# Kernel optimization log

Measured on AMD Instinct MI355X. Metric: run time of the kernel, lower is better.

The kernel has to match this reference:

```python
import jax, jax.numpy as jnp
import numpy as np

NUM_HEADS = 16
NEG_INF = -1e9  # matches torch source's -1000000000.0 additive mask
ROPE_BASE = 10000.0


def _rope(t):
    """Rotary position embedding, half-rotation form. t: [B, H, S, D]."""
    D = t.shape[-1]
    S = t.shape[2]
    inv_freq = 1.0 / (ROPE_BASE ** (jnp.arange(0, D, 2, dtype=jnp.float32) / D))  # [D/2]
    pos = jnp.arange(S, dtype=jnp.float32)
    freqs = pos[:, None] * inv_freq[None, :]          # [S, D/2]
    cos = jnp.cos(freqs)[None, None]                  # [1,1,S,D/2]
    sin = jnp.sin(freqs)[None, None]
    t1, t2 = t[..., : D // 2], t[..., D // 2 :]
    return jnp.concatenate([t1 * cos - t2 * sin, t1 * sin + t2 * cos], axis=-1)


def setup_inputs() -> dict:
    key = jax.random.key(0)
    kx, kq, kk, kv, ko = jax.random.split(key, 5)
    B, S, Dm = 2, 2048, 1024
    w_scale = 0.02
    return {
        "x": jax.random.normal(kx, (B, S, Dm), dtype=jnp.float32),
        "attention_mask": jnp.ones((B, S), dtype=jnp.float32),
        "Wq": jax.random.normal(kq, (Dm, Dm), dtype=jnp.float32) * w_scale,
        "Wk": jax.random.normal(kk, (Dm, Dm), dtype=jnp.float32) * w_scale,
        "Wv": jax.random.normal(kv, (Dm, Dm), dtype=jnp.float32) * w_scale,
        "Wo": jax.random.normal(ko, (Dm, Dm), dtype=jnp.float32) * w_scale,
    }


def reference(x, attention_mask, Wq, Wk, Wv, Wo):
    B, S, Dm = x.shape
    H = NUM_HEADS
    Hd = Dm // H

    def to_heads(t):  # [B,S,Dm] -> [B,H,S,Hd]
        return t.reshape(B, S, H, Hd).transpose(0, 2, 1, 3)

    q = _rope(to_heads(x @ Wq))
    k = _rope(to_heads(x @ Wk))
    v = to_heads(x @ Wv)

    scaling = 1.0 / np.sqrt(Hd).astype(np.float32)
    scores = jnp.einsum("bhqd,bhkd->bhqk", q, k) * scaling  # [B,H,S,S]

    # causal additive mask (triu of -1e9 above diagonal), as in apply_masking
    causal = jnp.triu(jnp.full((S, S), NEG_INF, dtype=scores.dtype), k=1)
    # padding mask: (1 - mask) * -1e9 broadcast to [B,1,1,S]
    amask = (1.0 - attention_mask)[:, None, None, :] * NEG_INF
    scores = scores + causal[None, None] + amask

    weights = jax.nn.softmax(scores, axis=-1)
    out = jnp.einsum("bhqk,bhkd->bhqd", weights, v)  # [B,H,S,Hd]
    out = out.transpose(0, 2, 1, 3).reshape(B, S, Dm)
    return out @ Wo
```

## Files before the change

kernel.cpp:

```cpp
#include <hip/hip_runtime.h>

typedef unsigned short u16;
typedef unsigned int u32;
typedef __attribute__((ext_vector_type(8))) short short8;
typedef __attribute__((ext_vector_type(4))) short s4v;
typedef __attribute__((ext_vector_type(4))) float f32x4;

#define S_LEN 2048
#define NH 16
#define HD 64
#define DM 1024

#if __has_builtin(__builtin_amdgcn_mfma_f32_16x16x16_bf16)
#define MFMA_K16(a, b, c) __builtin_amdgcn_mfma_f32_16x16x16_bf16(a, b, c, 0, 0, 0)
#else
#define MFMA_K16(a, b, c) __builtin_amdgcn_mfma_f32_16x16x16bf16_1k(a, b, c, 0, 0, 0)
#endif

__device__ __forceinline__ u16 f2bf(float f) {
    union { float f; u32 u; } v; v.f = f;
    u32 u = v.u;
    u32 r = u + 0x7fffu + ((u >> 16) & 1u);
    return (u16)(r >> 16);
}
__device__ __forceinline__ float bf2f(u16 h) {
    union { u32 u; float f; } v; v.u = ((u32)h) << 16;
    return v.f;
}

__device__ __forceinline__ u32 cvtpk_bf16(float lo, float hi) {
    u32 r;
    asm("v_cvt_pk_bf16_f32 %0, %1, %2" : "=v"(r) : "v"(lo), "v"(hi));
    return r;
}

__device__ __forceinline__ void load_lds16(const u16* g, u16* l) {
    __builtin_amdgcn_global_load_lds((const __attribute__((address_space(1))) void*)g,
                                     (__attribute__((address_space(3))) void*)l, 16, 0, 0);
}

__global__ __launch_bounds__(256) void cvt_bf16(const float* __restrict__ in, u16* __restrict__ out, int n) {
    int i = (blockIdx.x * 256 + threadIdx.x) * 4;
    if (i < n) {
        float4 v = *(const float4*)(in + i);
        ushort4 o;
        o.x = f2bf(v.x); o.y = f2bf(v.y); o.z = f2bf(v.z); o.w = f2bf(v.w);
        *(ushort4*)(out + i) = o;
    }
}

__global__ __launch_bounds__(256) void transpose_w4(const float* __restrict__ W0, const float* __restrict__ W1,
                                                    const float* __restrict__ W2, const float* __restrict__ W3,
                                                    u16* __restrict__ T0, u16* __restrict__ T1,
                                                    u16* __restrict__ T2, u16* __restrict__ T3) {
    __shared__ float tile[32][33];
    int z = blockIdx.z;
    const float* W = (z == 0) ? W0 : (z == 1) ? W1 : (z == 2) ? W2 : W3;
    u16* Wt = (z == 0) ? T0 : (z == 1) ? T1 : (z == 2) ? T2 : T3;
    int tx = threadIdx.x, ty = threadIdx.y;
    int k0 = blockIdx.y * 32, n0 = blockIdx.x * 32;
    #pragma unroll
    for (int j = 0; j < 32; j += 8)
        tile[ty + j][tx] = W[(size_t)(k0 + ty + j) * DM + n0 + tx];
    __syncthreads();
    #pragma unroll
    for (int j = 0; j < 32; j += 8)
        Wt[(size_t)(n0 + ty + j) * DM + k0 + tx] = f2bf(tile[tx][ty + j]);
}

template<int MODE, int NI>
__global__ __launch_bounds__(256) void gemm128(const u16* __restrict__ A, const u16* __restrict__ Bt,
                                               u16* __restrict__ Qh, u16* __restrict__ Kh,
                                               u16* __restrict__ Vh, float* __restrict__ Cf) {
    __shared__ u16 Al[128 * 32];
    __shared__ u16 Bl[NI * 32 * 32];
    const int K = DM;
    int tid = threadIdx.x;
    int wave = tid >> 6, lane = tid & 63, g = lane >> 4, ln = lane & 15;
    int wm = (wave >> 1) * 64, wn = (wave & 1) * (NI * 16);
    size_t mb0 = (size_t)blockIdx.y * 128, nb0 = (size_t)blockIdx.x * (NI * 32);

    f32x4 acc[4][NI];
    #pragma unroll
    for (int i = 0; i < 4; i++)
        #pragma unroll
        for (int j = 0; j < NI; j++)
            acc[i][j] = (f32x4){0.f, 0.f, 0.f, 0.f};

    const u16* Ag = A + (mb0 + wave * 32 + (lane >> 2)) * K + (lane & 3) * 8;
    u16* Alw = Al + wave * 1024;
    const u16* Bg;
    u16* Blw;
    if (NI == 4) {
        Bg = Bt + (nb0 + wave * 32 + (lane >> 2)) * K + (lane & 3) * 8;
        Blw = Bl + wave * 1024;
    } else {
        Bg = Bt + (nb0 + wave * 16 + (lane >> 2)) * K + (lane & 3) * 8;
        Blw = Bl + wave * 512;
    }

    for (int k0 = 0; k0 < K; k0 += 32) {
        __syncthreads();
        #pragma unroll
        for (int c = 0; c < 2; c++)
            load_lds16(Ag + (size_t)c * 16 * K + k0, Alw + c * 512);
        if (NI == 4) {
            #pragma unroll
            for (int c = 0; c < 2; c++)
                load_lds16(Bg + (size_t)c * 16 * K + k0, Blw + c * 512);
        } else {
            load_lds16(Bg + k0, Blw);
        }
        __syncthreads();
        short8 af[4], bf[NI];
        #pragma unroll
        for (int i = 0; i < 4; i++)
            af[i] = *(const short8*)&Al[(wm + i * 16 + ln) * 32 + g * 8];
        #pragma unroll
        for (int i = 0; i < NI; i++)
            bf[i] = *(const short8*)&Bl[(wn + i * 16 + ln) * 32 + g * 8];
        #pragma unroll
        for (int mi = 0; mi < 4; mi++)
            #pragma unroll
            for (int ni = 0; ni < NI; ni++)
                acc[mi][ni] = __builtin_amdgcn_mfma_f32_16x16x32_bf16(af[mi], bf[ni], acc[mi][ni], 0, 0, 0);
    }

    if (MODE == 1) {
        #pragma unroll
        for (int mi = 0; mi < 4; mi++)
            #pragma unroll
            for (int ni = 0; ni < NI; ni++)
                #pragma unroll
                for (int r = 0; r < 4; r++) {
                    int m = (int)mb0 + wm + mi * 16 + g * 4 + r;
                    int n = (int)nb0 + wn + ni * 16 + ln;
                    Cf[(size_t)m * DM + n] = acc[mi][ni][r];
                }
    } else {
        int nbase = (int)nb0 + wn;
        int which = nbase >> 10;
        int h = (nbase & (DM - 1)) >> 6;
        if (which < 2) {
            u16* dst = (which == 0) ? Qh : Kh;
            float inv0 = exp2f(-0.4152408746976557f * (float)ln);
            float inv1 = exp2f(-0.4152408746976557f * (float)(16 + ln));
            #pragma unroll
            for (int mi = 0; mi < 4; mi++) {
                #pragma unroll
                for (int r = 0; r < 4; r++) {
                    int m = (int)mb0 + wm + mi * 16 + g * 4 + r;
                    int b = m >> 11, s = m & (S_LEN - 1);
                    float fs = (float)s;
                    float sn0, cs0, sn1, cs1;
                    __sincosf(fs * inv0, &sn0, &cs0);
                    __sincosf(fs * inv1, &sn1, &cs1);
                    float a0 = acc[mi][0][r], a1 = acc[mi][1][r];
                    float a2 = acc[mi][2][r], a3 = acc[mi][3][r];
                    size_t base = ((size_t)(b * NH + h) * S_LEN + s) * HD;
                    dst[base + ln]      = f2bf(a0 * cs0 - a2 * sn0);
                    dst[base + 16 + ln] = f2bf(a1 * cs1 - a3 * sn1);
                    dst[base + 32 + ln] = f2bf(a0 * sn0 + a2 * cs0);
                    dst[base + 48 + ln] = f2bf(a1 * sn1 + a3 * cs1);
                }
            }
        } else {
            #pragma unroll
            for (int mi = 0; mi < 4; mi++) {
                #pragma unroll
                for (int r = 0; r < 4; r++) {
                    int m = (int)mb0 + wm + mi * 16 + g * 4 + r;
                    int b = m >> 11, s = m & (S_LEN - 1);
                    size_t base = ((size_t)(b * NH + h) * S_LEN + s) * HD;
                    #pragma unroll
                    for (int ni = 0; ni < 4; ni++)
                        Vh[base + ni * 16 + ln] = f2bf(acc[mi][ni][r]);
                }
            }
        }
    }
}

__global__ __launch_bounds__(256) void vtrans(const u16* __restrict__ Vh, u16* __restrict__ Vt) {
    __shared__ u16 t[64][70];
    int tid = threadIdx.x;
    int s0 = blockIdx.x * 64, bh = blockIdx.y;
    int r = tid >> 2, c = (tid & 3) * 8;
    const u16* src = Vh + ((size_t)bh * S_LEN + s0) * HD;
    *(short8*)&t[r][c]      = *(const short8*)(src + (size_t)r * HD + c);
    *(short8*)&t[r][c + 32] = *(const short8*)(src + (size_t)r * HD + c + 32);
    __syncthreads();
    u16* dst = Vt + ((size_t)bh * HD + r) * S_LEN + s0;
    short8 o0, o1;
    #pragma unroll
    for (int j = 0; j < 8; j++) {
        o0[j] = (short)t[c + j][r];
        o1[j] = (short)t[c + 32 + j][r];
    }
    *(short8*)(dst + c)      = o0;
    *(short8*)(dst + c + 32) = o1;
}

__global__ __launch_bounds__(512, 4) void flash_kernel(const u16* __restrict__ Qh, const u16* __restrict__ Kh,
                                                       const u16* __restrict__ Vt, const float* __restrict__ amask,
                                                       u16* __restrict__ Op0, u16* __restrict__ Op1,
                                                       u16* __restrict__ Op2, u16* __restrict__ Op3,
                                                       float* __restrict__ L0, float* __restrict__ L1,
                                                       float* __restrict__ L2, float* __restrict__ L3) {
    __shared__ u16 Kl[2][64 * 64];
    __shared__ u16 Vl[2][64 * 64];
    __shared__ float Ml[2][64];
    int tid = threadIdx.x;
    int wave = tid >> 6, lane = tid & 63, g = lane >> 4, ln = lane & 15;
    int qblk = 15 - ((int)blockIdx.x >> 2);
    int sp = blockIdx.x & 3;
    int bh = blockIdx.y;
    int b = bh >> 4, h = bh & (NH - 1);
    int q0 = qblk * 128 + wave * 16;
    int qv = q0 + ln;
    const u16* Qb = Qh + (size_t)bh * (S_LEN * HD);
    const u16* Kb = Kh + (size_t)bh * (S_LEN * HD);
    const u16* Vb = Vt + (size_t)bh * (S_LEN * HD);
    const float* am = amask + b * S_LEN;

    short8 qa0 = *(const short8*)(Qb + (size_t)(q0 + ln) * HD + g * 8);
    short8 qa1 = *(const short8*)(Qb + (size_t)(q0 + ln) * HD + 32 + g * 8);

    f32x4 O[4];
    #pragma unroll
    for (int i = 0; i < 4; i++) O[i] = (f32x4){0.f, 0.f, 0.f, 0.f};
    float lsum = 0.f;
    const float SCL = 0.125f * 1.4426950408889634f;
    const float MSCL = -1.4426950408889634e9f;

    int T = 2 * qblk + 2;
    int srow = tid >> 3, scid = tid & 7, s7 = srow & 7;
    int stoff = srow * 64 + ((scid ^ s7) * 8);
    const u16* KgP = Kb + (size_t)srow * HD + scid * 8;
    const u16* VgP = Vb + (size_t)srow * S_LEN + scid * 8;
    bool vswap = (wave & 1);

    int l7 = ln & 7;
    int kc0 = (g ^ l7) * 8;
    int kc1 = ((4 + g) ^ l7) * 8;
    int rbq = ln * 64;
    int vcoff[4];
    #pragma unroll
    for (int n0 = 0; n0 < 4; n0++)
        vcoff[n0] = (((n0 * 2 + (g >> 1)) ^ l7) * 8) + ((((g & 1) ^ (ln >> 3)) & 1) * 4);

    short8 kR = *(const short8*)(KgP + (size_t)(sp * 64) * HD);
    short8 vR = *(const short8*)(VgP + sp * 64);
    float mR = 0.f;
    if (tid < 64) mR = (1.0f - am[sp * 64 + tid]) * MSCL;
    int cur = 0;

    for (int kt = sp; kt < T; kt += 4) {
        int kbase = kt * 64;
        short8 vS = vR;
        if (vswap) vS = __builtin_shufflevector(vR, vR, 4, 5, 6, 7, 0, 1, 2, 3);
        *(short8*)(Kl[cur] + stoff) = kR;
        *(short8*)(Vl[cur] + stoff) = vS;
        if (tid < 64) Ml[cur][tid] = mR;
        __syncthreads();

        if (kt + 4 < T) {
            kR = *(const short8*)(KgP + (size_t)(kbase + 256) * HD);
            vR = *(const short8*)(VgP + (kbase + 256));
            if (tid < 64) mR = (1.0f - am[kbase + 256 + tid]) * MSCL;
        }

        const u16* Klc = Kl[cur];
        const u16* Vlc = Vl[cur];
        bool needmask = (kbase + 63 > q0);
        u32 pk[4][2];

        #pragma unroll
        for (int n0 = 0; n0 < 4; n0++) {
            const u16* kr = Klc + (n0 * 16) * 64 + rbq;
            short8 kb0 = *(const short8*)(kr + kc0);
            short8 kb1 = *(const short8*)(kr + kc1);
            f32x4 sv = (f32x4){0.f, 0.f, 0.f, 0.f};
            sv = __builtin_amdgcn_mfma_f32_16x16x32_bf16(kb0, qa0, sv, 0, 0, 0);
            sv = __builtin_amdgcn_mfma_f32_16x16x32_bf16(kb1, qa1, sv, 0, 0, 0);
            f32x4 mkv = *(f32x4*)&Ml[cur][n0 * 16 + g * 4];
            int keyb = kbase + n0 * 16 + g * 4;
            float p[4];
            #pragma unroll
            for (int r = 0; r < 4; r++) {
                float s2 = sv[r] * SCL + mkv[r];
                if (needmask && (keyb + r > qv)) s2 = -1.0e9f;
                p[r] = exp2f(s2);
                lsum += p[r];
            }
            pk[n0][0] = cvtpk_bf16(p[0], p[1]);
            pk[n0][1] = cvtpk_bf16(p[2], p[3]);
        }

        __builtin_amdgcn_s_setprio(1);
        #pragma unroll
        for (int t = 0; t < 4; t++) {
            const u16* vr = Vlc + (t * 16) * 64 + rbq;
            #pragma unroll
            for (int n0 = 0; n0 < 4; n0++) {
                s4v va = *(const s4v*)(vr + vcoff[n0]);
                union { u32 u[2]; s4v v; } pb;
                pb.u[0] = pk[n0][0];
                pb.u[1] = pk[n0][1];
                O[t] = MFMA_K16(va, pb.v, O[t]);
            }
        }
        __builtin_amdgcn_s_setprio(0);
        cur ^= 1;
    }

    lsum += __shfl_xor(lsum, 16, 64);
    lsum += __shfl_xor(lsum, 32, 64);
    u16* Od = (sp == 0) ? Op0 : (sp == 1) ? Op1 : (sp == 2) ? Op2 : Op3;
    float* Ld = (sp == 0) ? L0 : (sp == 1) ? L1 : (sp == 2) ? L2 : L3;
    if (lane < 16) Ld[(size_t)bh * S_LEN + q0 + ln] = lsum;
    size_t obase = (size_t)bh * (HD * S_LEN) + q0 + ln;
    #pragma unroll
    for (int t = 0; t < 4; t++)
        #pragma unroll
        for (int r = 0; r < 4; r++)
            Od[obase + (size_t)(t * 16 + g * 4 + r) * S_LEN] = f2bf(O[t][r]);
}

__global__ __launch_bounds__(256) void flash_reduce(const u16* __restrict__ Op0, const u16* __restrict__ Op1,
                                                    const u16* __restrict__ Op2, const u16* __restrict__ Op3,
                                                    const float* __restrict__ L0, const float* __restrict__ L1,
                                                    const float* __restrict__ L2, const float* __restrict__ L3,
                                                    u16* __restrict__ attn) {
    __shared__ float t[64][65];
    int tid = threadIdx.x;
    int qt = blockIdx.x, bh = blockIdx.y;
    int b = bh >> 4, h = bh & (NH - 1);
    #pragma unroll
    for (int it = 0; it < 2; it++) {
        int idx = tid + it * 256;
        int d = idx >> 3, c = (idx & 7) * 8;
        size_t off = (size_t)bh * (HD * S_LEN) + (size_t)d * S_LEN + qt * 64 + c;
        short8 a0 = *(const short8*)(Op0 + off);
        short8 a1 = *(const short8*)(Op1 + off);
        short8 a2 = *(const short8*)(Op2 + off);
        short8 a3 = *(const short8*)(Op3 + off);
        #pragma unroll
        for (int j = 0; j < 8; j++)
            t[d][c + j] = bf2f((u16)a0[j]) + bf2f((u16)a1[j]) + bf2f((u16)a2[j]) + bf2f((u16)a3[j]);
    }
    __syncthreads();
    int qr = tid >> 2, dc = (tid & 3) * 16;
    int qg = qt * 64 + qr;
    size_t li = (size_t)bh * S_LEN + qg;
    float inv = 1.0f / (L0[li] + L1[li] + L2[li] + L3[li]);
    short8 o0, o1;
    #pragma unroll
    for (int j = 0; j < 8; j++) {
        o0[j] = (short)f2bf(t[dc + j][qr] * inv);
        o1[j] = (short)f2bf(t[dc + 8 + j][qr] * inv);
    }
    u16* dst = attn + ((size_t)b * S_LEN + qg) * DM + h * HD + dc;
    *(short8*)dst = o0;
    *(short8*)(dst + 8) = o1;
}

extern "C" void kernel_launch(void* const* d_in, const int* in_sizes, int n_in,
                              void* d_out, int out_size, void* d_ws, size_t ws_size,
                              hipStream_t stream) {
    const float* x     = (const float*)d_in[0];
    const float* amask = (const float*)d_in[1];
    const float* Wq    = (const float*)d_in[2];
    const float* Wk    = (const float*)d_in[3];
    const float* Wv    = (const float*)d_in[4];
    const float* Wo    = (const float*)d_in[5];
    float* out = (float*)d_out;
    char* ws = (char*)d_ws;

    u16* x_bf   = (u16*)(ws);
    u16* Op1    = (u16*)(ws);
    u16* Wqkv_t = (u16*)(ws + 8388608);
    float* L0   = (float*)(ws + 8388608);
    float* L1   = (float*)(ws + 8650752);
    float* L2   = (float*)(ws + 8912896);
    float* L3   = (float*)(ws + 9175040);
    u16* Wo_t   = (u16*)(ws + 14680064);
    u16* Qh     = (u16*)(ws + 16777216);
    u16* Kh     = (u16*)(ws + 25165824);
    u16* Vt     = (u16*)(ws + 33554432);
    u16* attnF  = (u16*)(ws + 33554432);
    u16* Vh     = (u16*)(ws + 41943040);
    u16* Op0    = (u16*)(ws + 41943040);
    u16* Op2    = (u16*)d_out;
    u16* Op3    = (u16*)d_out + 4194304;

    cvt_bf16<<<4096, 256, 0, stream>>>(x, x_bf, 2 * S_LEN * DM);

    transpose_w4<<<dim3(32, 32, 4), dim3(32, 8), 0, stream>>>(
        Wq, Wk, Wv, Wo, Wqkv_t, Wqkv_t + 1048576, Wqkv_t + 2097152, Wo_t);

    gemm128<0, 4><<<dim3(24, 32), 256, 0, stream>>>(x_bf, Wqkv_t, Qh, Kh, Vh, nullptr);

    vtrans<<<dim3(32, 2 * NH), 256, 0, stream>>>(Vh, Vt);

    flash_kernel<<<dim3(64, 2 * NH), 512, 0, stream>>>(Qh, Kh, Vt, amask,
                                                       Op0, Op1, Op2, Op3, L0, L1, L2, L3);

    flash_reduce<<<dim3(32, 2 * NH), 256, 0, stream>>>(Op0, Op1, Op2, Op3,
                                                       L0, L1, L2, L3, attnF);

    gemm128<1, 2><<<dim3(16, 32), 256, 0, stream>>>(attnF, Wo_t, nullptr, nullptr, nullptr, out);
}
```

Baseline: 225.0 us.

## Double queries per wave in flash kernel and precompute padding mask

Each wave now processes 32 query rows instead of 16, so every K/V tile staged in LDS feeds twice as many MFMAs. The block's query tile grows to 256 and the grid halves, and waves whose rows all sit above a key tile skip it under the causal mask. The padding-mask transform moves into vtrans, which writes it to a global buffer read directly by the flash kernel, removing the per-tile LDS mask staging. This raises register pressure (launch bounds drop from 4 to 3 blocks per CU) and leaves fewer blocks, with more causal imbalance within each block.

```diff
diff --git a/kernel.cpp b/kernel.cpp
--- a/kernel.cpp
+++ b/kernel.cpp
@@ -10,6 +10,7 @@
 #define NH 16
 #define HD 64
 #define DM 1024
+#define MSCL_C (-1.4426950408889634e9f)
 
 #if __has_builtin(__builtin_amdgcn_mfma_f32_16x16x16_bf16)
 #define MFMA_K16(a, b, c) __builtin_amdgcn_mfma_f32_16x16x16_bf16(a, b, c, 0, 0, 0)
@@ -181,10 +182,15 @@
     }
 }
 
-__global__ __launch_bounds__(256) void vtrans(const u16* __restrict__ Vh, u16* __restrict__ Vt) {
+__global__ __launch_bounds__(256) void vtrans(const u16* __restrict__ Vh, u16* __restrict__ Vt,
+                                              const float* __restrict__ amask, float* __restrict__ Mg) {
     __shared__ u16 t[64][70];
     int tid = threadIdx.x;
     int s0 = blockIdx.x * 64, bh = blockIdx.y;
+    if (bh == 0) {
+        int idx = blockIdx.x * 256 + tid;
+        if (idx < 2 * S_LEN) Mg[idx] = (1.0f - amask[idx]) * MSCL_C;
+    }
     int r = tid >> 2, c = (tid & 3) * 8;
     const u16* src = Vh + ((size_t)bh * S_LEN + s0) * HD;
     *(short8*)&t[r][c]      = *(const short8*)(src + (size_t)r * HD + c);
@@ -201,39 +207,39 @@
     *(short8*)(dst + c + 32) = o1;
 }
 
-__global__ __launch_bounds__(512, 4) void flash_kernel(const u16* __restrict__ Qh, const u16* __restrict__ Kh,
-                                                       const u16* __restrict__ Vt, const float* __restrict__ amask,
+__global__ __launch_bounds__(512, 3) void flash_kernel(const u16* __restrict__ Qh, const u16* __restrict__ Kh,
+                                                       const u16* __restrict__ Vt, const float* __restrict__ Mg,
                                                        u16* __restrict__ Op0, u16* __restrict__ Op1,
                                                        u16* __restrict__ Op2, u16* __restrict__ Op3,
                                                        float* __restrict__ L0, float* __restrict__ L1,
                                                        float* __restrict__ L2, float* __restrict__ L3) {
     __shared__ u16 Kl[2][64 * 64];
     __shared__ u16 Vl[2][64 * 64];
-    __shared__ float Ml[2][64];
     int tid = threadIdx.x;
     int wave = tid >> 6, lane = tid & 63, g = lane >> 4, ln = lane & 15;
-    int qblk = 15 - ((int)blockIdx.x >> 2);
+    int qblk = 7 - ((int)blockIdx.x >> 2);
     int sp = blockIdx.x & 3;
     int bh = blockIdx.y;
-    int b = bh >> 4, h = bh & (NH - 1);
-    int q0 = qblk * 128 + wave * 16;
-    int qv = q0 + ln;
+    int b = bh >> 4;
+    int q0 = qblk * 256 + wave * 32;
+    int qvA = q0 + ln, qvB = q0 + 16 + ln;
     const u16* Qb = Qh + (size_t)bh * (S_LEN * HD);
     const u16* Kb = Kh + (size_t)bh * (S_LEN * HD);
     const u16* Vb = Vt + (size_t)bh * (S_LEN * HD);
-    const float* am = amask + b * S_LEN;
+    const float* Mb = Mg + b * S_LEN;
 
     short8 qa0 = *(const short8*)(Qb + (size_t)(q0 + ln) * HD + g * 8);
     short8 qa1 = *(const short8*)(Qb + (size_t)(q0 + ln) * HD + 32 + g * 8);
-
-    f32x4 O[4];
-    #pragma unroll
-    for (int i = 0; i < 4; i++) O[i] = (f32x4){0.f, 0.f, 0.f, 0.f};
-    float lsum = 0.f;
+    short8 qb0 = *(const short8*)(Qb + (size_t)(q0 + 16 + ln) * HD + g * 8);
+    short8 qb1 = *(const short8*)(Qb + (size_t)(q0 + 16 + ln) * HD + 32 + g * 8);
+
+    f32x4 O[8];
+    #pragma unroll
+    for (int i = 0; i < 8; i++) O[i] = (f32x4){0.f, 0.f, 0.f, 0.f};
+    float lsa = 0.f, lsb = 0.f;
     const float SCL = 0.125f * 1.4426950408889634f;
-    const float MSCL = -1.4426950408889634e9f;
-
-    int T = 2 * qblk + 2;
+
+    int T = 4 * qblk + 4;
     int srow = tid >> 3, scid = tid & 7, s7 = srow & 7;
     int stoff = srow * 64 + ((scid ^ s7) * 8);
     const u16* KgP = Kb + (size_t)srow * HD + scid * 8;
@@ -251,8 +257,6 @@
 
     short8 kR = *(const short8*)(KgP + (size_t)(sp * 64) * HD);
     short8 vR = *(const short8*)(VgP + sp * 64);
-    float mR = 0.f;
-    if (tid < 64) mR = (1.0f - am[sp * 64 + tid]) * MSCL;
     int cur = 0;
 
     for (int kt = sp; kt < T; kt += 4) {
@@ -261,70 +265,94 @@
         if (vswap) vS = __builtin_shufflevector(vR, vR, 4, 5, 6, 7, 0, 1, 2, 3);
         *(short8*)(Kl[cur] + stoff) = kR;
         *(short8*)(Vl[cur] + stoff) = vS;
-        if (tid < 64) Ml[cur][tid] = mR;
         __syncthreads();
 
         if (kt + 4 < T) {
             kR = *(const short8*)(KgP + (size_t)(kbase + 256) * HD);
             vR = *(const short8*)(VgP + (kbase + 256));
-            if (tid < 64) mR = (1.0f - am[kbase + 256 + tid]) * MSCL;
         }
 
-        const u16* Klc = Kl[cur];
-        const u16* Vlc = Vl[cur];
-        bool needmask = (kbase + 63 > q0);
-        u32 pk[4][2];
-
-        #pragma unroll
-        for (int n0 = 0; n0 < 4; n0++) {
-            const u16* kr = Klc + (n0 * 16) * 64 + rbq;
-            short8 kb0 = *(const short8*)(kr + kc0);
-            short8 kb1 = *(const short8*)(kr + kc1);
-            f32x4 sv = (f32x4){0.f, 0.f, 0.f, 0.f};
-            sv = __builtin_amdgcn_mfma_f32_16x16x32_bf16(kb0, qa0, sv, 0, 0, 0);
-            sv = __builtin_amdgcn_mfma_f32_16x16x32_bf16(kb1, qa1, sv, 0, 0, 0);
-            f32x4 mkv = *(f32x4*)&Ml[cur][n0 * 16 + g * 4];
-            int keyb = kbase + n0 * 16 + g * 4;
-            float p[4];
-            #pragma unroll
-            for (int r = 0; r < 4; r++) {
-                float s2 = sv[r] * SCL + mkv[r];
-                if (needmask && (keyb + r > qv)) s2 = -1.0e9f;
-                p[r] = exp2f(s2);
-                lsum += p[r];
+        if (kbase <= q0 + 31) {
+            const u16* Klc = Kl[cur];
+            const u16* Vlc = Vl[cur];
+            f32x4 mk[4];
+            #pragma unroll
+            for (int n0 = 0; n0 < 4; n0++)
+                mk[n0] = *(const f32x4*)(Mb + kbase + n0 * 16 + g * 4);
+            bool nmA = (kbase + 63 > q0);
+            bool nmB = (kbase + 63 > q0 + 16);
+            u32 pkA[4][2], pkB[4][2];
+
+            #pragma unroll
+            for (int n0 = 0; n0 < 4; n0++) {
+                const u16* kr = Klc + (n0 * 16) * 64 + rbq;
+                short8 kb0 = *(const short8*)(kr + kc0);
+                short8 kb1 = *(const short8*)(kr + kc1);
+                f32x4 sva = (f32x4){0.f, 0.f, 0.f, 0.f};
+                sva = __builtin_amdgcn_mfma_f32_16x16x32_bf16(kb0, qa0, sva, 0, 0, 0);
+                sva = __builtin_amdgcn_mfma_f32_16x16x32_bf16(kb1, qa1, sva, 0, 0, 0);
+                f32x4 svb = (f32x4){0.f, 0.f, 0.f, 0.f};
+                svb = __builtin_amdgcn_mfma_f32_16x16x32_bf16(kb0, qb0, svb, 0, 0, 0);
+                svb = __builtin_amdgcn_mfma_f32_16x16x32_bf16(kb1, qb1, svb, 0, 0, 0);
+                int keyb = kbase + n0 * 16 + g * 4;
+                float pa[4], pb[4];
+                #pragma unroll
+                for (int r = 0; r < 4; r++) {
+                    float s2 = sva[r] * SCL + mk[n0][r];
+                    if (nmA && (keyb + r > qvA)) s2 = -1.0e9f;
+                    pa[r] = exp2f(s2);
+                    lsa += pa[r];
+                }
+                #pragma unroll
+                for (int r = 0; r < 4; r++) {
+                    float s2 = svb[r] * SCL + mk[n0][r];
+                    if (nmB && (keyb + r > qvB)) s2 = -1.0e9f;
+                    pb[r] = exp2f(s2);
+                    lsb += pb[r];
+                }
+                pkA[n0][0] = cvtpk_bf16(pa[0], pa[1]);
+                pkA[n0][1] = cvtpk_bf16(pa[2], pa[3]);
+                pkB[n0][0] = cvtpk_bf16(pb[0], pb[1]);
+                pkB[n0][1] = cvtpk_bf16(pb[2], pb[3]);
             }
-            pk[n0][0] = cvtpk_bf16(p[0], p[1]);
-            pk[n0][1] = cvtpk_bf16(p[2], p[3]);
+
+            __builtin_amdgcn_s_setprio(1);
+            #pragma unroll
+            for (int t = 0; t < 4; t++) {
+                const u16* vr = Vlc + (t * 16) * 64 + rbq;
+                #pragma unroll
+                for (int n0 = 0; n0 < 4; n0++) {
+                    s4v va = *(const s4v*)(vr + vcoff[n0]);
+                    union { u32 u[2]; s4v v; } pba, pbb;
+                    pba.u[0] = pkA[n0][0]; pba.u[1] = pkA[n0][1];
+                    pbb.u[0] = pkB[n0][0]; pbb.u[1] = pkB[n0][1];
+                    O[t]     = MFMA_K16(va, pba.v, O[t]);
+                    O[4 + t] = MFMA_K16(va, pbb.v, O[4 + t]);
+                }
+            }
+            __builtin_amdgcn_s_setprio(0);
         }
-
-        __builtin_amdgcn_s_setprio(1);
-        #pragma unroll
-        for (int t = 0; t < 4; t++) {
-            const u16* vr = Vlc + (t * 16) * 64 + rbq;
-            #pragma unroll
-            for (int n0 = 0; n0 < 4; n0++) {
-                s4v va = *(const s4v*)(vr + vcoff[n0]);
-                union { u32 u[2]; s4v v; } pb;
-                pb.u[0] = pk[n0][0];
-                pb.u[1] = pk[n0][1];
-                O[t] = MFMA_K16(va, pb.v, O[t]);
-            }
-        }
-        __builtin_amdgcn_s_setprio(0);
         cur ^= 1;
     }
 
-    lsum += __shfl_xor(lsum, 16, 64);
-    lsum += __shfl_xor(lsum, 32, 64);
+    lsa += __shfl_xor(lsa, 16, 64);
+    lsa += __shfl_xor(lsa, 32, 64);
+    lsb += __shfl_xor(lsb, 16, 64);
+    lsb += __shfl_xor(lsb, 32, 64);
     u16* Od = (sp == 0) ? Op0 : (sp == 1) ? Op1 : (sp == 2) ? Op2 : Op3;
     float* Ld = (sp == 0) ? L0 : (sp == 1) ? L1 : (sp == 2) ? L2 : L3;
-    if (lane < 16) Ld[(size_t)bh * S_LEN + q0 + ln] = lsum;
+    if (lane < 16) {
+        Ld[(size_t)bh * S_LEN + q0 + ln] = lsa;
+        Ld[(size_t)bh * S_LEN + q0 + 16 + ln] = lsb;
+    }
     size_t obase = (size_t)bh * (HD * S_LEN) + q0 + ln;
     #pragma unroll
     for (int t = 0; t < 4; t++)
         #pragma unroll
-        for (int r = 0; r < 4; r++)
-            Od[obase + (size_t)(t * 16 + g * 4 + r) * S_LEN] = f2bf(O[t][r]);
+        for (int r = 0; r < 4; r++) {
+            Od[obase + (size_t)(t * 16 + g * 4 + r) * S_LEN]      = f2bf(O[t][r]);
+            Od[obase + 16 + (size_t)(t * 16 + g * 4 + r) * S_LEN] = f2bf(O[4 + t][r]);
+        }
 }
 
 __global__ __launch_bounds__(256) void flash_reduce(const u16* __restrict__ Op0, const u16* __restrict__ Op1,
@@ -384,6 +412,7 @@
     float* L1   = (float*)(ws + 8650752);
     float* L2   = (float*)(ws + 8912896);
     float* L3   = (float*)(ws + 9175040);
+    float* Mg   = (float*)(ws + 9437184);
     u16* Wo_t   = (u16*)(ws + 14680064);
     u16* Qh     = (u16*)(ws + 16777216);
     u16* Kh     = (u16*)(ws + 25165824);
@@ -401,9 +430,9 @@
 
     gemm128<0, 4><<<dim3(24, 32), 256, 0, stream>>>(x_bf, Wqkv_t, Qh, Kh, Vh, nullptr);
 
-    vtrans<<<dim3(32, 2 * NH), 256, 0, stream>>>(Vh, Vt);
-
-    flash_kernel<<<dim3(64, 2 * NH), 512, 0, stream>>>(Qh, Kh, Vt, amask,
+    vtrans<<<dim3(32, 2 * NH), 256, 0, stream>>>(Vh, Vt, amask, Mg);
+
+    flash_kernel<<<dim3(32, 2 * NH), 512, 0, stream>>>(Qh, Kh, Vt, Mg,
                                                        Op0, Op1, Op2, Op3, L0, L1, L2, L3);
 
     flash_reduce<<<dim3(32, 2 * NH), 256, 0, stream>>>(Op0, Op1, Op2, Op3,
```

Result: slower. 248.2 us (+10.3%).
